# Performance work log

Measured on AMD Instinct MI355X. Metric: run time of the kernel, lower is better.

The kernel has to match this reference:

```python
import jax, jax.numpy as jnp
import numpy as np

NUM_HEADS = 8
LN_EPS = 1e-5


def _ln(x, g, b):
    mu = x.mean(-1, keepdims=True)
    xc = x - mu
    v = (xc * xc).mean(-1, keepdims=True)
    return xc * jax.lax.rsqrt(v + LN_EPS) * g + b


def setup_inputs() -> dict:
    key = jax.random.key(0)
    B, T, D, NI, NT = 16, 512, 256, 85, 77
    L, FF, TH = 2, 1024, 32
    ks = iter(jax.random.split(key, 40))
    def nrm(shape, std):
        return jax.random.normal(next(ks), shape, jnp.float32) * std
    inp = {
        'img_tokens': nrm((B, NI, D), 1.0),
        'text_tokens': nrm((B, NT, D), 1.0),
        'task_tokens': nrm((T, D), 0.02),
        'type_task': nrm((D,), 0.02),
        'type_img': nrm((D,), 0.02),
        'type_txt': nrm((D,), 0.02),
        'in_ln_g': jnp.ones((D,), jnp.float32), 'in_ln_b': jnp.zeros((D,), jnp.float32),
        'Wqkv': nrm((L, 3 * D, D), 1.0 / np.sqrt(D)), 'bqkv': jnp.zeros((L, 3 * D), jnp.float32),
        'Wo': nrm((L, D, D), 1.0 / np.sqrt(D)), 'bo': jnp.zeros((L, D), jnp.float32),
        'ln1_g': jnp.ones((L, D), jnp.float32), 'ln1_b': jnp.zeros((L, D), jnp.float32),
        'ln2_g': jnp.ones((L, D), jnp.float32), 'ln2_b': jnp.zeros((L, D), jnp.float32),
        'W1': nrm((L, FF, D), 1.0 / np.sqrt(D)), 'b1': jnp.zeros((L, FF), jnp.float32),
        'W2': nrm((L, D, FF), 1.0 / np.sqrt(FF)), 'b2': jnp.zeros((L, D), jnp.float32),
        'out_ln_g': jnp.ones((D,), jnp.float32), 'out_ln_b': jnp.zeros((D,), jnp.float32),
        'tw1': nrm((T, TH, D), 1.0 / np.sqrt(D)), 'tb1': jnp.zeros((T, TH), jnp.float32),
        'tw2': nrm((T, TH), 1.0 / np.sqrt(TH)), 'tb2': jnp.zeros((T,), jnp.float32),
        'text_mask': jnp.arange(NT)[None, :] < jax.random.randint(next(ks), (B, 1), 10, NT + 1),
        'labels': jax.random.randint(next(ks), (B, T), -1, 2),
    }
    return inp


def reference(img_tokens, text_tokens, task_tokens, type_task, type_img, type_txt,
              in_ln_g, in_ln_b, Wqkv, bqkv, Wo, bo, ln1_g, ln1_b, ln2_g, ln2_b,
              W1, b1, W2, b2, out_ln_g, out_ln_b, tw1, tb1, tw2, tb2,
              text_mask, labels):
    B, NI, D = img_tokens.shape
    T = task_tokens.shape[0]
    L = Wqkv.shape[0]
    hd = D // NUM_HEADS
    available = labels != -1                                   # (B, T)
    n_avail = available.sum(axis=1)                            # (B,)
    # Route B: stable-sort available task ids to the front (permutation per row)
    order = jnp.argsort((~available).astype(jnp.int32), axis=1, stable=True)  # (B, T)
    task_toks = task_tokens[order] + type_task                 # (B, T, D)
    seq = jnp.concatenate([task_toks, img_tokens + type_img, text_tokens + type_txt], axis=1)
    seq = _ln(seq, in_ln_g, in_ln_b)
    task_pad = jnp.arange(T)[None, :] >= n_avail[:, None]
    pad = jnp.concatenate([task_pad, jnp.zeros((B, NI), bool), ~text_mask], axis=1)
    bias = jnp.where(pad, -1e9, 0.0).astype(seq.dtype)[:, None, None, :]  # key-padding mask
    scale = 1.0 / np.sqrt(hd)
    S = seq.shape[1]
    for l in range(L):  # pre-LN transformer encoder layers (eval mode)
        h = _ln(seq, ln1_g[l], ln1_b[l])
        qkv = h @ Wqkv[l].T + bqkv[l]
        q, k, v = jnp.split(qkv, 3, axis=-1)
        q = q.reshape(B, S, NUM_HEADS, hd)
        k = k.reshape(B, S, NUM_HEADS, hd)
        v = v.reshape(B, S, NUM_HEADS, hd)
        scores = jnp.einsum('bqhd,bkhd->bhqk', q, k) * scale + bias
        attn = jax.nn.softmax(scores, axis=-1)
        o = jnp.einsum('bhqk,bkhd->bqhd', attn, v).reshape(B, S, D)
        seq = seq + o @ Wo[l].T + bo[l]
        h2 = _ln(seq, ln2_g[l], ln2_b[l])
        seq = seq + jax.nn.gelu(h2 @ W1[l].T + b1[l], approximate=False) @ W2[l].T + b2[l]
    task_out = _ln(seq[:, :T], out_ln_g, out_ln_b)             # (B, T, D)
    # undo the per-row permutation so task t's token sits at column t, then
    # apply all per-task towers as one grouped matmul (MoE dispatch/combine)
    y = jnp.zeros_like(task_out).at[jnp.arange(B)[:, None], order].set(task_out)
    hsz = jax.nn.relu(jnp.einsum('btd,thd->bth', y, tw1) + tb1[None])
    out = jnp.einsum('bth,th->bt', hsz, tw2) + tb2[None]
    return jnp.where(available, out, jnp.zeros((), out.dtype))
```

## Files before the change

kernel.cpp:

```cpp
#include <hip/hip_runtime.h>
#include <hip/hip_bf16.h>
#include <math.h>

constexpr int B_  = 16;
constexpr int T_  = 512;
constexpr int D_  = 256;
constexpr int NI_ = 85;
constexpr int NT_ = 77;
constexpr int S_  = T_ + NI_ + NT_;
constexpr int M_  = B_ * S_;
constexpr int FF_ = 1024;
constexpr int TH_ = 32;
constexpr int NH_ = 8;
constexpr int KT_ = 704;
constexpr int NKT_ = KT_ / 64;

constexpr float MASK_NEG = -30000.0f;

constexpr int N_FT = 26;
constexpr int OFF_[N_FT + 1] = {
    0,
    348160,
    663552,
    794624,
    794880,
    795136,
    795392,
    795648,
    795904,
    1189120,
    1190656,
    1321728,
    1322240,
    1322752,
    1323264,
    1323776,
    1324288,
    1848576,
    1850624,
    2374912,
    2375424,
    2375680,
    2375936,
    6570240,
    6586624,
    6603008,
    6603520
};
constexpr int TOTAL_ELEMS = OFF_[N_FT];
constexpr int CONV_BLOCKS = (TOTAL_ELEMS + 511) / 512;

typedef __attribute__((ext_vector_type(8))) short bfrag;
typedef __attribute__((ext_vector_type(4))) float f32x4;

__device__ inline float bf2f(__hip_bfloat16 x) { return __bfloat162float(x); }
__device__ inline __hip_bfloat16 f2bf(float x) { return __float2bfloat16(x); }
__device__ inline float wsum64(float v) {
    #pragma unroll
    for (int m = 32; m >= 1; m >>= 1) v += __shfl_xor(v, m, 64);
    return v;
}
__device__ inline bool is_f32_mode(const void* ln_g_raw) {
    return (*(const unsigned int*)ln_g_raw) == 0x3F800000u;
}

__device__ inline bool tile_dead(int m0, int m1, const int* __restrict__ n_avail) {
    int b = m0 / S_;
    int base = b * S_;
    return (m0 >= base + n_avail[b]) && (m1 <= base + T_);
}

__device__ inline void gload_lds16(const __hip_bfloat16* g, __hip_bfloat16* l) {
#if defined(__has_builtin) && __has_builtin(__builtin_amdgcn_global_load_lds)
    __builtin_amdgcn_global_load_lds(
        (const __attribute__((address_space(1))) unsigned int*)g,
        (__attribute__((address_space(3))) unsigned int*)l, 16, 0, 0);
#else
    *reinterpret_cast<uint4*>(l) = *reinterpret_cast<const uint4*>(g);
#endif
}

__device__ inline float gelu_f(float v) {
    return 0.5f * v * (1.f + erff(v * 0.70710678118654752f));
}

struct Ptrs { const void* p[N_FT]; };

__global__ __launch_bounds__(512) void k_init(Ptrs ptrs, __hip_bfloat16* __restrict__ canon,
                                              const int* __restrict__ labels,
                                              int* __restrict__ inv,
                                              int* __restrict__ n_avail) {
    if (blockIdx.x < CONV_BLOCKS) {
        int idx = blockIdx.x * 512 + threadIdx.x;
        if (idx >= TOTAL_ELEMS) return;
        bool f32 = is_f32_mode(ptrs.p[6]);
        int t = 0;
        #pragma unroll
        for (int i = 1; i < N_FT; i++) if (idx >= OFF_[i]) t = i;
        int local = idx - OFF_[t];
        if (f32) canon[idx] = f2bf(((const float*)ptrs.p[t])[local]);
        else     canon[idx] = ((const __hip_bfloat16*)ptrs.p[t])[local];
    } else {
        __shared__ int sc[T_];
        int b = blockIdx.x - CONV_BLOCKS, t = threadIdx.x;
        int av = (labels[b * T_ + t] != -1) ? 1 : 0;
        sc[t] = av;
        __syncthreads();
        for (int off = 1; off < T_; off <<= 1) {
            int v = sc[t];
            int u = (t >= off) ? sc[t - off] : 0;
            __syncthreads();
            sc[t] = v + u;
            __syncthreads();
        }
        int incl  = sc[t];
        int excl  = incl - av;
        int total = sc[T_ - 1];
        inv[b * T_ + t] = av ? excl : (total + (t - excl));
        if (t == 0) n_avail[b] = total;
    }
}

__global__ void k_build(const __hip_bfloat16* __restrict__ img,
                        const __hip_bfloat16* __restrict__ txt,
                        const __hip_bfloat16* __restrict__ task,
                        const __hip_bfloat16* __restrict__ ty_task,
                        const __hip_bfloat16* __restrict__ ty_img,
                        const __hip_bfloat16* __restrict__ ty_txt,
                        const __hip_bfloat16* __restrict__ g,
                        const __hip_bfloat16* __restrict__ bln,
                        const __hip_bfloat16* __restrict__ g1,
                        const __hip_bfloat16* __restrict__ b1,
                        const void* __restrict__ text_mask,
                        const int* __restrict__ inv,
                        const int* __restrict__ n_avail,
                        float* __restrict__ seq,
                        __hip_bfloat16* __restrict__ h1,
                        float* __restrict__ bias) {
    int blk = blockIdx.x;
    int b = blk / S_, j = blk % S_;
    int lane = threadIdx.x;

    int dest;
    float bias_v;
    const __hip_bfloat16* src;
    const __hip_bfloat16* tvec;
    if (j < T_) {
        dest = inv[b * T_ + j];
        src = task + (size_t)j * D_;
        tvec = ty_task;
        bias_v = (dest >= n_avail[b]) ? MASK_NEG : 0.f;
    } else if (j < T_ + NI_) {
        dest = j;
        src = img + (size_t)(b * NI_ + (j - T_)) * D_;
        tvec = ty_img;
        bias_v = 0.f;
    } else {
        int x2 = j - T_ - NI_;
        dest = j;
        src = txt + (size_t)(b * NT_ + x2) * D_;
        tvec = ty_txt;
        const unsigned char* mb = (const unsigned char*)text_mask;
        bool is_byte = (mb[1] != 0);
        int mv = is_byte ? (int)mb[b * NT_ + x2]
                         : ((const int*)text_mask)[b * NT_ + x2];
        bias_v = mv ? 0.f : MASK_NEG;
    }

    float x[4];
    float s = 0.f, ss = 0.f;
    #pragma unroll
    for (int i = 0; i < 4; i++) {
        int d = lane * 4 + i;
        x[i] = bf2f(src[d]) + bf2f(tvec[d]);
        s += x[i];
        ss += x[i] * x[i];
    }
    s = wsum64(s);
    ss = wsum64(ss);
    float mean = s * (1.f / D_);
    float var  = ss * (1.f / D_) - mean * mean;
    float r    = rsqrtf(fmaxf(var, 0.f) + 1e-5f);

    float y[4];
    float s2 = 0.f, ss2 = 0.f;
    float* orow = seq + ((size_t)b * S_ + dest) * D_;
    #pragma unroll
    for (int i = 0; i < 4; i++) {
        int d = lane * 4 + i;
        y[i] = (x[i] - mean) * r * bf2f(g[d]) + bf2f(bln[d]);
        orow[d] = y[i];
        s2 += y[i];
        ss2 += y[i] * y[i];
    }
    s2 = wsum64(s2);
    ss2 = wsum64(ss2);
    float mean2 = s2 * (1.f / D_);
    float var2  = ss2 * (1.f / D_) - mean2 * mean2;
    float r2    = rsqrtf(fmaxf(var2, 0.f) + 1e-5f);
    __hip_bfloat16 tmp[4];
    #pragma unroll
    for (int i = 0; i < 4; i++) {
        int d = lane * 4 + i;
        tmp[i] = f2bf((y[i] - mean2) * r2 * bf2f(g1[d]) + bf2f(b1[d]));
    }
    *reinterpret_cast<uint2*>(h1 + ((size_t)b * S_ + dest) * D_ + lane * 4) =
        *reinterpret_cast<uint2*>(tmp);
    if (lane == 0) bias[b * S_ + dest] = bias_v;
}

template <int GELU>
__global__ __launch_bounds__(256) void k_gemm(const __hip_bfloat16* __restrict__ A,
                                              const __hip_bfloat16* __restrict__ W,
                                              const __hip_bfloat16* __restrict__ bias,
                                              __hip_bfloat16* __restrict__ Cout,
                                              const int* __restrict__ n_avail,
                                              int Mm, int N, int K) {
    constexpr int HALF = 12288;
    __shared__ __align__(16) __hip_bfloat16 Sh[2 * HALF];
    __hip_bfloat16* Es = Sh;

    int m0 = blockIdx.x * 64;
    if (tile_dead(m0, m0 + 64, n_avail)) return;
    int n0 = blockIdx.y * 128;
    int tid = threadIdx.x;
    int w = tid >> 6, lane = tid & 63;
    int lrow = lane & 15, quad = lane >> 4;
    int swz = lrow & 7;

    f32x4 acc[8] = {};

    int kq = (((tid & 7) ^ ((tid >> 3) & 7)) * 8);
    int arow = tid >> 3;
    const __hip_bfloat16* Ar0 = A + (size_t)min(m0 + arow,      Mm - 1) * K + kq;
    const __hip_bfloat16* Ar1 = A + (size_t)min(m0 + arow + 32, Mm - 1) * K + kq;
    const __hip_bfloat16* Wr[4];
    #pragma unroll
    for (int i = 0; i < 4; i++)
        Wr[i] = W + (size_t)(n0 + ((tid + i * 256) >> 3)) * K + kq;

    const int nsteps = K >> 6;

    {
        __hip_bfloat16* As0 = Sh;
        __hip_bfloat16* Ws0 = Sh + 4096;
        gload_lds16(Ar0, As0 + tid * 8);
        gload_lds16(Ar1, As0 + (tid + 256) * 8);
        #pragma unroll
        for (int i = 0; i < 4; i++) gload_lds16(Wr[i], Ws0 + (tid + i * 256) * 8);
    }
    __syncthreads();

    for (int ks = 0; ks < nsteps; ks++) {
        int curo = (ks & 1) * HALF;
        if (ks + 1 < nsteps) {
            int k1 = (ks + 1) << 6;
            __hip_bfloat16* Asn = Sh + (HALF - curo);
            __hip_bfloat16* Wsn = Asn + 4096;
            gload_lds16(Ar0 + k1, Asn + tid * 8);
            gload_lds16(Ar1 + k1, Asn + (tid + 256) * 8);
            #pragma unroll
            for (int i = 0; i < 4; i++) gload_lds16(Wr[i] + k1, Wsn + (tid + i * 256) * 8);
        }
        __hip_bfloat16* Asc = Sh + curo;
        __hip_bfloat16* Wsc = Asc + 4096;
        #pragma unroll
        for (int ko = 0; ko < 2; ko++) {
            int unit = ((ko * 4 + quad) ^ swz) << 3;
            bfrag af = *reinterpret_cast<const bfrag*>(&Asc[(w * 16 + lrow) * 64 + unit]);
            #pragma unroll
            for (int nt = 0; nt < 8; nt++) {
                bfrag bf = *reinterpret_cast<const bfrag*>(&Wsc[(nt * 16 + lrow) * 64 + unit]);
                acc[nt] = __builtin_amdgcn_mfma_f32_16x16x32_bf16(af, bf, acc[nt], 0, 0, 0);
            }
        }
        __syncthreads();
    }

    #pragma unroll
    for (int nt = 0; nt < 8; nt++) {
        int col = nt * 16 + lrow;
        float bv = bf2f(bias[n0 + col]);
        #pragma unroll
        for (int rg = 0; rg < 4; rg++) {
            int row = w * 16 + quad * 4 + rg;
            float v = acc[nt][rg] + bv;
            if (GELU) v = gelu_f(v);
            Es[row * 136 + col] = f2bf(v);
        }
    }
    __syncthreads();

    #pragma unroll
    for (int i = 0; i < 4; i++) {
        int c = tid + i * 256;
        int row = c >> 4, off = (c & 15) * 8;
        int gm = m0 + row;
        if (gm < Mm) {
            uint4 v4 = *reinterpret_cast<const uint4*>(&Es[row * 136 + off]);
            *reinterpret_cast<uint4*>(&Cout[(size_t)gm * N + n0 + off]) = v4;
        }
    }
}

template <int LNOUT>
__global__ __launch_bounds__(256) void k_ffnmega(const __hip_bfloat16* __restrict__ A,
                                                 const __hip_bfloat16* __restrict__ Wop,
                                                 const __hip_bfloat16* __restrict__ bop,
                                                 const __hip_bfloat16* __restrict__ ln2g,
                                                 const __hip_bfloat16* __restrict__ ln2b,
                                                 const __hip_bfloat16* __restrict__ W1p,
                                                 const __hip_bfloat16* __restrict__ b1p,
                                                 const __hip_bfloat16* __restrict__ W2p,
                                                 const __hip_bfloat16* __restrict__ b2p,
                                                 float* __restrict__ seq,
                                                 const __hip_bfloat16* __restrict__ g1n,
                                                 const __hip_bfloat16* __restrict__ b1n,
                                                 __hip_bfloat16* __restrict__ lnout,
                                                 const int* __restrict__ n_avail) {
    constexpr int PT_OFF  = 0;
    constexpr int WST_OFF = 4096;
    constexpr int HT_OFF  = 20480;
    constexpr int ESTRIDE = 260;
    __shared__ __align__(16) __hip_bfloat16 Sh[28672];

    int m0 = blockIdx.x * 32;
    if (tile_dead(m0, m0 + 32, n_avail)) return;
    int tid = threadIdx.x;
    int w = tid >> 6, lane = tid & 63;
    int lrow = lane & 15, quad = lane >> 4;
    int swz = lrow & 7;
    int kq = ((tid & 7) ^ ((tid >> 3) & 7)) * 8;

    f32x4 acc[2][4] = {};
    {
        const __hip_bfloat16* Ar = A + (size_t)(m0 + (tid >> 3)) * 256 + kq;
        __hip_bfloat16* As = Sh;
        __hip_bfloat16* Ws = Sh + 2048;
        for (int ks = 0; ks < 4; ks++) {
            int k0 = ks << 6;
            if (ks) __syncthreads();
            gload_lds16(Ar + k0, As + tid * 8);
            #pragma unroll
            for (int i = 0; i < 8; i++)
                gload_lds16(Wop + (size_t)((tid + i * 256) >> 3) * 256 + k0 + kq,
                            Ws + (tid + i * 256) * 8);
            __syncthreads();
            #pragma unroll
            for (int ko = 0; ko < 2; ko++) {
                int unit = ((ko * 4 + quad) ^ swz) << 3;
                bfrag af[2], bf[4];
                #pragma unroll
                for (int mt = 0; mt < 2; mt++)
                    af[mt] = *reinterpret_cast<const bfrag*>(&As[(mt * 16 + lrow) * 64 + unit]);
                #pragma unroll
                for (int nt = 0; nt < 4; nt++)
                    bf[nt] = *reinterpret_cast<const bfrag*>(&Ws[(w * 64 + nt * 16 + lrow) * 64 + unit]);
                #pragma unroll
                for (int mt = 0; mt < 2; mt++)
                    #pragma unroll
                    for (int nt = 0; nt < 4; nt++)
                        acc[mt][nt] = __builtin_amdgcn_mfma_f32_16x16x32_bf16(af[mt], bf[nt], acc[mt][nt], 0, 0, 0);
            }
        }
        __syncthreads();
    }

    float* Es = (float*)Sh;
    #pragma unroll
    for (int nt = 0; nt < 4; nt++) {
        int col = w * 64 + nt * 16 + lrow;
        float bv = bf2f(bop[col]);
        #pragma unroll
        for (int mt = 0; mt < 2; mt++)
            #pragma unroll
            for (int rg = 0; rg < 4; rg++)
                Es[(mt * 16 + quad * 4 + rg) * ESTRIDE + col] = acc[mt][nt][rg] + bv;
    }
    __syncthreads();

    int row = tid >> 3, part = tid & 7;
    size_t gm = (size_t)(m0 + row);
    const float* seqrow = seq + gm * 256 + part * 32;
    float t[32];
    float s = 0.f, ss = 0.f;
    #pragma unroll
    for (int j = 0; j < 8; j++) {
        float4 e  = *reinterpret_cast<const float4*>(&Es[row * ESTRIDE + part * 32 + j * 4]);
        float4 r4 = *reinterpret_cast<const float4*>(&seqrow[j * 4]);
        float v0 = e.x + r4.x, v1 = e.y + r4.y, v2 = e.z + r4.z, v3 = e.w + r4.w;
        t[j * 4 + 0] = v0; t[j * 4 + 1] = v1; t[j * 4 + 2] = v2; t[j * 4 + 3] = v3;
        s += v0 + v1 + v2 + v3;
        ss += v0 * v0 + v1 * v1 + v2 * v2 + v3 * v3;
    }
    #pragma unroll
    for (int mm = 4; mm >= 1; mm >>= 1) {
        s  += __shfl_xor(s,  mm, 8);
        ss += __shfl_xor(ss, mm, 8);
    }
    {
        float mean = s * (1.f / 256);
        float var  = ss * (1.f / 256) - mean * mean;
        float r    = rsqrtf(fmaxf(var, 0.f) + 1e-5f);
        __hip_bfloat16* Ht = Sh + HT_OFF;
        #pragma unroll
        for (int jj = 0; jj < 4; jj++) {
            __hip_bfloat16 hb[8];
            #pragma unroll
            for (int k = 0; k < 8; k++) {
                int col = part * 32 + jj * 8 + k;
                hb[k] = f2bf((t[jj * 8 + k] - mean) * r * bf2f(ln2g[col]) + bf2f(ln2b[col]));
            }
            int unit = (part * 4 + jj) ^ (row & 7);
            *reinterpret_cast<uint4*>(&Ht[row * 256 + unit * 8]) =
                *reinterpret_cast<const uint4*>(hb);
        }
    }
    __syncthreads();

    f32x4 acc2[2][4] = {};
    __hip_bfloat16* Wst = Sh + WST_OFF;
    __hip_bfloat16* Pt  = Sh + PT_OFF;
    __hip_bfloat16* Ht  = Sh + HT_OFF;

    for (int c = 0; c < 8; c++) {
        int ff0 = c << 7;
        f32x4 pacc[2][2] = {};
        for (int ks = 0; ks < 4; ks++) {
            if (c | ks) __syncthreads();
            #pragma unroll
            for (int i = 0; i < 4; i++) {
                int u = tid + i * 256;
                gload_lds16(W1p + (size_t)(ff0 + (u >> 3)) * 256 + (ks << 6) + kq,
                            Wst + u * 8);
            }
            __syncthreads();
            #pragma unroll
            for (int ko = 0; ko < 2; ko++) {
                int hunit = ((ks * 8 + ko * 4 + quad) ^ swz) << 3;
                int wunit = ((ko * 4 + quad) ^ swz) << 3;
                bfrag af[2], bf[2];
                #pragma unroll
                for (int mt = 0; mt < 2; mt++)
                    af[mt] = *reinterpret_cast<const bfrag*>(&Ht[(mt * 16 + lrow) * 256 + hunit]);
                #pragma unroll
                for (int nt = 0; nt < 2; nt++)
                    bf[nt] = *reinterpret_cast<const bfrag*>(&Wst[(w * 32 + nt * 16 + lrow) * 64 + wunit]);
                #pragma unroll
                for (int mt = 0; mt < 2; mt++)
                    #pragma unroll
                    for (int nt = 0; nt < 2; nt++)
                        pacc[mt][nt] = __builtin_amdgcn_mfma_f32_16x16x32_bf16(af[mt], bf[nt], pacc[mt][nt], 0, 0, 0);
            }
        }
        __syncthreads();

        #pragma unroll
        for (int mt = 0; mt < 2; mt++)
            #pragma unroll
            for (int nt = 0; nt < 2; nt++)
                #pragma unroll
                for (int rg = 0; rg < 4; rg++) {
                    int prow = mt * 16 + quad * 4 + rg;
                    int pcol = w * 32 + nt * 16 + lrow;
                    float v = pacc[mt][nt][rg] + bf2f(b1p[ff0 + pcol]);
                    v = gelu_f(v);
                    int unit = (pcol >> 3) ^ (prow & 7);
                    Pt[prow * 128 + unit * 8 + (pcol & 7)] = f2bf(v);
                }

        for (int ks2 = 0; ks2 < 2; ks2++) {
            if (ks2) __syncthreads();
            #pragma unroll
            for (int i = 0; i < 8; i++) {
                int u = tid + i * 256;
                gload_lds16(W2p + (size_t)(u >> 3) * 1024 + ff0 + (ks2 << 6) + kq,
                            Wst + u * 8);
            }
            __syncthreads();
            #pragma unroll
            for (int ko = 0; ko < 2; ko++) {
                int punit = ((ks2 * 8 + ko * 4 + quad) ^ swz) << 3;
                int wunit = ((ko * 4 + quad) ^ swz) << 3;
                bfrag af2[2], bf2v[4];
                #pragma unroll
                for (int mt = 0; mt < 2; mt++)
                    af2[mt] = *reinterpret_cast<const bfrag*>(&Pt[(mt * 16 + lrow) * 128 + punit]);
                #pragma unroll
                for (int nt = 0; nt < 4; nt++)
                    bf2v[nt] = *reinterpret_cast<const bfrag*>(&Wst[(w * 64 + nt * 16 + lrow) * 64 + wunit]);
                #pragma unroll
                for (int mt = 0; mt < 2; mt++)
                    #pragma unroll
                    for (int nt = 0; nt < 4; nt++)
                        acc2[mt][nt] = __builtin_amdgcn_mfma_f32_16x16x32_bf16(af2[mt], bf2v[nt], acc2[mt][nt], 0, 0, 0);
            }
        }
    }
    __syncthreads();

    float* Es2 = (float*)Sh;
    #pragma unroll
    for (int nt = 0; nt < 4; nt++) {
        int col = w * 64 + nt * 16 + lrow;
        float bv = bf2f(b2p[col]);
        #pragma unroll
        for (int mt = 0; mt < 2; mt++)
            #pragma unroll
            for (int rg = 0; rg < 4; rg++)
                Es2[(mt * 16 + quad * 4 + rg) * ESTRIDE + col] = acc2[mt][nt][rg] + bv;
    }
    __syncthreads();

    float* seqw = seq + gm * 256 + part * 32;
    float s2 = 0.f, ss2 = 0.f;
    #pragma unroll
    for (int j = 0; j < 8; j++) {
        float4 e = *reinterpret_cast<const float4*>(&Es2[row * ESTRIDE + part * 32 + j * 4]);
        float v0 = t[j * 4 + 0] + e.x, v1 = t[j * 4 + 1] + e.y;
        float v2 = t[j * 4 + 2] + e.z, v3 = t[j * 4 + 3] + e.w;
        t[j * 4 + 0] = v0; t[j * 4 + 1] = v1; t[j * 4 + 2] = v2; t[j * 4 + 3] = v3;
        s2 += v0 + v1 + v2 + v3;
        ss2 += v0 * v0 + v1 * v1 + v2 * v2 + v3 * v3;
        *reinterpret_cast<float4*>(&seqw[j * 4]) = make_float4(v0, v1, v2, v3);
    }
    if (LNOUT) {
        #pragma unroll
        for (int mm = 4; mm >= 1; mm >>= 1) {
            s2  += __shfl_xor(s2,  mm, 8);
            ss2 += __shfl_xor(ss2, mm, 8);
        }
        float mean = s2 * (1.f / 256);
        float var  = ss2 * (1.f / 256) - mean * mean;
        float r    = rsqrtf(fmaxf(var, 0.f) + 1e-5f);
        __hip_bfloat16 ob[32];
        #pragma unroll
        for (int j = 0; j < 32; j++) {
            int col = part * 32 + j;
            ob[j] = f2bf((t[j] - mean) * r * bf2f(g1n[col]) + bf2f(b1n[col]));
        }
        #pragma unroll
        for (int j = 0; j < 4; j++)
            *reinterpret_cast<uint4*>(&lnout[gm * 256 + part * 32 + j * 8]) =
                *reinterpret_cast<const uint4*>(&ob[j * 8]);
    }
}

__global__ __launch_bounds__(256) void k_fattn(const __hip_bfloat16* __restrict__ qkv,
                                               const float* __restrict__ bias,
                                               const int* __restrict__ n_avail,
                                               __hip_bfloat16* __restrict__ out) {
    __shared__ __align__(16) __hip_bfloat16 Vt[2][32 * 72];
    __shared__ __align__(16) __hip_bfloat16 Ps[4][32 * 72];
    __shared__ float Bs[KT_];
    __shared__ int alive[NKT_];
    __shared__ int tlist[NKT_ + 1];
    __shared__ int nact_s;
    int b = blockIdx.z, h = blockIdx.y;
    int q0b = blockIdx.x * 128;
    if (q0b >= n_avail[b] && q0b + 128 <= T_) return;
    int tid = threadIdx.x;
    int wave = tid >> 6, lane = tid & 63;
    int lrow = lane & 15, quad = lane >> 4;
    int q0 = q0b + wave * 32;

    const float scale = 0.17677669529663687f;
    const __hip_bfloat16* base = qkv + (size_t)b * S_ * 768;
    const float* brow = bias + b * S_;

    if (tid < NKT_) alive[tid] = 0;
    __syncthreads();
    for (int i = tid; i < KT_; i += 256) {
        float v = (i < S_) ? brow[i] : MASK_NEG;
        Bs[i] = v;
        if (v != MASK_NEG) alive[i >> 6] = 1;
    }
    __syncthreads();
    if (tid == 0) {
        int n = 0;
        for (int t = 0; t < NKT_; t++) if (alive[t]) tlist[n++] = t;
        if (n == 0) { tlist[0] = 0; n = 1; }
        tlist[n] = tlist[n - 1];
        nact_s = n;
    }
    __syncthreads();
    int nact = nact_s;

    bfrag qf[2];
    {
        int qr0 = min(q0 + lrow, S_ - 1);
        int qr1 = min(q0 + 16 + lrow, S_ - 1);
        qf[0] = *reinterpret_cast<const bfrag*>(base + (size_t)qr0 * 768 + h * 32 + quad * 8);
        qf[1] = *reinterpret_cast<const bfrag*>(base + (size_t)qr1 * 768 + h * 32 + quad * 8);
    }

    bfrag ones_f;
    #pragma unroll
    for (int i = 0; i < 8; i++) ((short*)&ones_f)[i] = (short)0x3F80;

    float m[2][4];
    #pragma unroll
    for (int qh = 0; qh < 2; qh++)
        #pragma unroll
        for (int rg = 0; rg < 4; rg++) m[qh][rg] = -3e38f;
    f32x4 Lacc[2] = {};
    f32x4 O[2][2] = {};

    int skey = lane;
    int sd   = wave * 8;

    bfrag kf_cur[4], vv_cur;
    {
        int k0 = tlist[0] * 64;
        #pragma unroll
        for (int nt = 0; nt < 4; nt++) {
            int kr = min(k0 + nt * 16 + lrow, S_ - 1);
            kf_cur[nt] = *reinterpret_cast<const bfrag*>(base + (size_t)kr * 768 + 256 + h * 32 + quad * 8);
        }
        int kr = min(k0 + skey, S_ - 1);
        vv_cur = *reinterpret_cast<const bfrag*>(base + (size_t)kr * 768 + 512 + h * 32 + sd);
    }

    for (int i = 0; i < nact; i++) {
        int k0 = tlist[i] * 64;
        __hip_bfloat16* vb = Vt[i & 1];

        #pragma unroll
        for (int j = 0; j < 8; j++) vb[(sd + j) * 72 + skey] = ((const __hip_bfloat16*)&vv_cur)[j];
        __syncthreads();

        bfrag kf_nxt[4], vv_nxt;
        {
            int kb = tlist[i + 1] * 64;
            #pragma unroll
            for (int nt = 0; nt < 4; nt++) {
                int kr = min(kb + nt * 16 + lrow, S_ - 1);
                kf_nxt[nt] = *reinterpret_cast<const bfrag*>(base + (size_t)kr * 768 + 256 + h * 32 + quad * 8);
            }
            int kr = min(kb + skey, S_ - 1);
            vv_nxt = *reinterpret_cast<const bfrag*>(base + (size_t)kr * 768 + 512 + h * 32 + sd);
        }

        f32x4 sc[2][4];
        #pragma unroll
        for (int nt = 0; nt < 4; nt++) {
            float bv = Bs[k0 + nt * 16 + lrow];
            #pragma unroll
            for (int qh = 0; qh < 2; qh++) {
                f32x4 z = {};
                sc[qh][nt] = __builtin_amdgcn_mfma_f32_16x16x32_bf16(qf[qh], kf_cur[nt], z, 0, 0, 0);
                #pragma unroll
                for (int rg = 0; rg < 4; rg++) sc[qh][nt][rg] = sc[qh][nt][rg] * scale + bv;
            }
        }

        #pragma unroll
        for (int qh = 0; qh < 2; qh++) {
            float alpha[4];
            #pragma unroll
            for (int rg = 0; rg < 4; rg++) {
                float rm = fmaxf(fmaxf(sc[qh][0][rg], sc[qh][1][rg]), fmaxf(sc[qh][2][rg], sc[qh][3][rg]));
                #pragma unroll
                for (int mm2 = 1; mm2 <= 8; mm2 <<= 1) rm = fmaxf(rm, __shfl_xor(rm, mm2, 64));
                float mn = fmaxf(m[qh][rg], rm);
                alpha[rg] = __expf(m[qh][rg] - mn);
                m[qh][rg] = mn;
                #pragma unroll
                for (int nt = 0; nt < 4; nt++) sc[qh][nt][rg] = __expf(sc[qh][nt][rg] - mn);
            }
            #pragma unroll
            for (int rg = 0; rg < 4; rg++) {
                O[qh][0][rg] *= alpha[rg];
                O[qh][1][rg] *= alpha[rg];
                Lacc[qh][rg] *= alpha[rg];
            }
            #pragma unroll
            for (int nt = 0; nt < 4; nt++)
                #pragma unroll
                for (int rg = 0; rg < 4; rg++)
                    Ps[wave][(qh * 16 + quad * 4 + rg) * 72 + nt * 16 + lrow] = f2bf(sc[qh][nt][rg]);
        }

        #pragma unroll
        for (int qh = 0; qh < 2; qh++) {
            bfrag ap0 = *reinterpret_cast<const bfrag*>(&Ps[wave][(qh * 16 + lrow) * 72 + quad * 8]);
            bfrag ap1 = *reinterpret_cast<const bfrag*>(&Ps[wave][(qh * 16 + lrow) * 72 + 32 + quad * 8]);
            #pragma unroll
            for (int dt = 0; dt < 2; dt++) {
                bfrag bv0 = *reinterpret_cast<const bfrag*>(&vb[(dt * 16 + lrow) * 72 + quad * 8]);
                bfrag bv1 = *reinterpret_cast<const bfrag*>(&vb[(dt * 16 + lrow) * 72 + 32 + quad * 8]);
                O[qh][dt] = __builtin_amdgcn_mfma_f32_16x16x32_bf16(ap0, bv0, O[qh][dt], 0, 0, 0);
                O[qh][dt] = __builtin_amdgcn_mfma_f32_16x16x32_bf16(ap1, bv1, O[qh][dt], 0, 0, 0);
            }
            Lacc[qh] = __builtin_amdgcn_mfma_f32_16x16x32_bf16(ap0, ones_f, Lacc[qh], 0, 0, 0);
            Lacc[qh] = __builtin_amdgcn_mfma_f32_16x16x32_bf16(ap1, ones_f, Lacc[qh], 0, 0, 0);
        }

        #pragma unroll
        for (int nt = 0; nt < 4; nt++) kf_cur[nt] = kf_nxt[nt];
        vv_cur = vv_nxt;
    }

    #pragma unroll
    for (int qh = 0; qh < 2; qh++)
        #pragma unroll
        for (int rg = 0; rg < 4; rg++) {
            int qrow = q0 + qh * 16 + quad * 4 + rg;
            if (qrow < S_) {
                float invl = 1.f / Lacc[qh][rg];
                #pragma unroll
                for (int dt = 0; dt < 2; dt++)
                    out[((size_t)b * S_ + qrow) * D_ + h * 32 + dt * 16 + lrow] = f2bf(O[qh][dt][rg] * invl);
            }
        }
}

__global__ __launch_bounds__(256) void k_final(const float* __restrict__ seq,
                                               const int* __restrict__ inv,
                                               const int* __restrict__ labels,
                                               const __hip_bfloat16* __restrict__ g,
                                               const __hip_bfloat16* __restrict__ bb,
                                               const __hip_bfloat16* __restrict__ tw1,
                                               const __hip_bfloat16* __restrict__ tb1,
                                               const __hip_bfloat16* __restrict__ tw2,
                                               const __hip_bfloat16* __restrict__ tb2,
                                               const void* __restrict__ ln_g_raw,
                                               void* __restrict__ out) {
    int idx = blockIdx.x;
    int t = idx >> 4, b = idx & 15;
    int tid = threadIdx.x;
    bool f32o = is_f32_mode(ln_g_raw);

    int lab = labels[b * T_ + t];
    if (lab == -1) {
        if (tid == 0) {
            if (f32o) ((float*)out)[b * T_ + t] = 0.f;
            else      ((__hip_bfloat16*)out)[b * T_ + t] = f2bf(0.f);
        }
        return;
    }

    __shared__ float y[D_];
    __shared__ float hb[TH_];
    __shared__ float rs[4], rq[4];

    int row = inv[b * T_ + t];
    float x = seq[((size_t)b * S_ + row) * D_ + tid];
    float s1 = wsum64(x);
    float s2 = wsum64(x * x);
    int w = tid >> 6, lane = tid & 63;
    if (lane == 0) { rs[w] = s1; rq[w] = s2; }
    __syncthreads();
    float fs = rs[0] + rs[1] + rs[2] + rs[3];
    float fq = rq[0] + rq[1] + rq[2] + rq[3];
    float mean = fs * (1.f / D_);
    float var  = fq * (1.f / D_) - mean * mean;
    float r    = rsqrtf(fmaxf(var, 0.f) + 1e-5f);
    y[tid] = (x - mean) * r * bf2f(g[tid]) + bf2f(bb[tid]);
    __syncthreads();

    int hh = tid >> 3, part = tid & 7;
    const uint4* w4 = reinterpret_cast<const uint4*>(tw1 + ((size_t)t * TH_ + hh) * D_ + part * 32);
    float acc = 0.f;
    #pragma unroll
    for (int i = 0; i < 4; i++) {
        uint4 kv = w4[i];
        unsigned int wd[4] = {kv.x, kv.y, kv.z, kv.w};
        #pragma unroll
        for (int j2 = 0; j2 < 4; j2++) {
            unsigned int lo = wd[j2] << 16, hi = wd[j2] & 0xffff0000u;
            float flo, fhi;
            __builtin_memcpy(&flo, &lo, 4);
            __builtin_memcpy(&fhi, &hi, 4);
            acc += y[part * 32 + i * 8 + j2 * 2] * flo;
            acc += y[part * 32 + i * 8 + j2 * 2 + 1] * fhi;
        }
    }
    #pragma unroll
    for (int mm = 4; mm >= 1; mm >>= 1) acc += __shfl_down(acc, mm, 8);
    if (part == 0) {
        float hz = acc + bf2f(tb1[t * TH_ + hh]);
        hz = fmaxf(hz, 0.f);
        hb[hh] = hz * bf2f(tw2[t * TH_ + hh]);
    }
    __syncthreads();
    if (tid == 0) {
        float o = bf2f(tb2[t]);
        #pragma unroll
        for (int i = 0; i < TH_; i++) o += hb[i];
        if (f32o) ((float*)out)[b * T_ + t] = o;
        else      ((__hip_bfloat16*)out)[b * T_ + t] = f2bf(o);
    }
}

extern "C" void kernel_launch(void* const* d_in, const int* in_sizes, int n_in,
                              void* d_out, int out_size, void* d_ws, size_t ws_size,
                              hipStream_t stream) {
    const void* tmask  = d_in[26];
    const int*  labels = (const int*)d_in[27];

    char* p = (char*)d_ws;
    auto alloc = [&](size_t bytes) {
        char* r = p;
        p += (bytes + 255) & ~size_t(255);
        return r;
    };
    __hip_bfloat16* canon  = (__hip_bfloat16*)alloc(sizeof(__hip_bfloat16) * (size_t)TOTAL_ELEMS);
    int*            inv     = (int*)alloc(sizeof(int) * B_ * T_);
    int*            n_avail = (int*)alloc(sizeof(int) * B_);
    float*          bias    = (float*)alloc(sizeof(float) * M_);
    float*          seqF    = (float*)alloc(sizeof(float) * (size_t)M_ * D_);
    __hip_bfloat16* bufA    = (__hip_bfloat16*)alloc(sizeof(__hip_bfloat16) * (size_t)M_ * D_);
    __hip_bfloat16* bufBig  = (__hip_bfloat16*)alloc(sizeof(__hip_bfloat16) * (size_t)M_ * FF_);

    Ptrs ptrs;
    for (int i = 0; i < N_FT; i++) ptrs.p[i] = d_in[i];
    hipLaunchKernelGGL(k_init, dim3(CONV_BLOCKS + B_), dim3(512), 0, stream,
                       ptrs, canon, labels, inv, n_avail);

    const __hip_bfloat16* img      = canon + OFF_[0];
    const __hip_bfloat16* txt      = canon + OFF_[1];
    const __hip_bfloat16* task     = canon + OFF_[2];
    const __hip_bfloat16* ty_task  = canon + OFF_[3];
    const __hip_bfloat16* ty_img   = canon + OFF_[4];
    const __hip_bfloat16* ty_txt   = canon + OFF_[5];
    const __hip_bfloat16* in_ln_g  = canon + OFF_[6];
    const __hip_bfloat16* in_ln_b  = canon + OFF_[7];
    const __hip_bfloat16* Wqkv     = canon + OFF_[8];
    const __hip_bfloat16* bqkv     = canon + OFF_[9];
    const __hip_bfloat16* Wo       = canon + OFF_[10];
    const __hip_bfloat16* bo       = canon + OFF_[11];
    const __hip_bfloat16* ln1_g    = canon + OFF_[12];
    const __hip_bfloat16* ln1_b    = canon + OFF_[13];
    const __hip_bfloat16* ln2_g    = canon + OFF_[14];
    const __hip_bfloat16* ln2_b    = canon + OFF_[15];
    const __hip_bfloat16* W1       = canon + OFF_[16];
    const __hip_bfloat16* b1       = canon + OFF_[17];
    const __hip_bfloat16* W2       = canon + OFF_[18];
    const __hip_bfloat16* b2       = canon + OFF_[19];
    const __hip_bfloat16* out_ln_g = canon + OFF_[20];
    const __hip_bfloat16* out_ln_b = canon + OFF_[21];
    const __hip_bfloat16* tw1      = canon + OFF_[22];
    const __hip_bfloat16* tb1      = canon + OFF_[23];
    const __hip_bfloat16* tw2      = canon + OFF_[24];
    const __hip_bfloat16* tb2      = canon + OFF_[25];

    hipLaunchKernelGGL(k_build, dim3(B_ * S_), dim3(64), 0, stream,
                       img, txt, task, ty_task, ty_img, ty_txt, in_ln_g, in_ln_b,
                       ln1_g, ln1_b, tmask, inv, n_avail, seqF, bufA, bias);

    const int mtiles = (M_ + 63) / 64;
    const int rtiles = M_ / 32;
    const int qtiles = (S_ + 127) / 128;

    for (int l = 0; l < 2; l++) {
        hipLaunchKernelGGL((k_gemm<0>), dim3(mtiles, 6), dim3(256), 0, stream,
                           bufA, Wqkv + (size_t)l * 3 * D_ * D_, bqkv + l * 3 * D_,
                           bufBig, n_avail, M_, 3 * D_, D_);
        hipLaunchKernelGGL(k_fattn, dim3(qtiles, NH_, B_), dim3(256), 0, stream,
                           bufBig, bias, n_avail, bufA);
        if (l == 0) {
            hipLaunchKernelGGL((k_ffnmega<1>), dim3(rtiles), dim3(256), 0, stream,
                               bufA,
                               Wo + (size_t)l * D_ * D_, bo + l * D_,
                               ln2_g + l * D_, ln2_b + l * D_,
                               W1 + (size_t)l * FF_ * D_, b1 + l * FF_,
                               W2 + (size_t)l * D_ * FF_, b2 + l * D_,
                               seqF, ln1_g + 1 * D_, ln1_b + 1 * D_, bufA, n_avail);
        } else {
            hipLaunchKernelGGL((k_ffnmega<0>), dim3(rtiles), dim3(256), 0, stream,
                               bufA,
                               Wo + (size_t)l * D_ * D_, bo + l * D_,
                               ln2_g + l * D_, ln2_b + l * D_,
                               W1 + (size_t)l * FF_ * D_, b1 + l * FF_,
                               W2 + (size_t)l * D_ * FF_, b2 + l * D_,
                               seqF, (const __hip_bfloat16*)nullptr,
                               (const __hip_bfloat16*)nullptr,
                               (__hip_bfloat16*)nullptr, n_avail);
        }
    }

    hipLaunchKernelGGL(k_final, dim3(T_ * B_), dim3(256), 0, stream,
                       seqF, inv, labels, out_ln_g, out_ln_b,
                       tw1, tb1, tw2, tb2, d_in[6], d_out);
}
```

Measured before the change: 366.1 us.

## Double-buffer weight staging in fused out-proj/FFN kernel to overlap loads with MFMA

Reworks the k_ffnmega weight staging into a uniform 128x64 tile loader with two LDS buffers. The next tile (Wo, W1 or W2) is prefetched while the current one feeds the MFMAs, which leaves one barrier per step instead of two. The A tile is loaded once into the Ht region, and the output-column mapping is split into two 128-column halves to match the smaller tiles. The cost is more, smaller stages and a more intricate buffer/barrier schedule, including the GELU-to-Pt handoff at the end of each W1 chunk.

```diff
diff --git a/kernel.cpp b/kernel.cpp
--- a/kernel.cpp
+++ b/kernel.cpp
@@ -318,7 +318,6 @@
                                                  const __hip_bfloat16* __restrict__ b1n,
                                                  __hip_bfloat16* __restrict__ lnout,
                                                  const int* __restrict__ n_avail) {
-    constexpr int PT_OFF  = 0;
     constexpr int WST_OFF = 4096;
     constexpr int HT_OFF  = 20480;
     constexpr int ESTRIDE = 260;
@@ -330,52 +329,70 @@
     int w = tid >> 6, lane = tid & 63;
     int lrow = lane & 15, quad = lane >> 4;
     int swz = lrow & 7;
-    int kq = ((tid & 7) ^ ((tid >> 3) & 7)) * 8;
-
+
+    __hip_bfloat16* Pt  = Sh;
+    __hip_bfloat16* Wst = Sh + WST_OFF;
+    __hip_bfloat16* Ht  = Sh + HT_OFF;
+
+    auto stageW = [&](const __hip_bfloat16* srcbase, int rowstride, __hip_bfloat16* dst) {
+        #pragma unroll
+        for (int i = 0; i < 4; i++) {
+            int u = tid + i * 256;
+            int r = u >> 3, c = u & 7;
+            gload_lds16(srcbase + (size_t)r * rowstride + ((c ^ (r & 7)) << 3), dst + u * 8);
+        }
+    };
+
+    #pragma unroll
+    for (int i = 0; i < 4; i++) {
+        int u = tid + i * 256;
+        int r = u >> 5, c = u & 31;
+        gload_lds16(A + (size_t)(m0 + r) * 256 + ((c ^ (r & 7)) << 3), Ht + u * 8);
+    }
+    stageW(Wop, 256, Wst);
+    __syncthreads();
+
+    int bufp = 0;
     f32x4 acc[2][4] = {};
-    {
-        const __hip_bfloat16* Ar = A + (size_t)(m0 + (tid >> 3)) * 256 + kq;
-        __hip_bfloat16* As = Sh;
-        __hip_bfloat16* Ws = Sh + 2048;
-        for (int ks = 0; ks < 4; ks++) {
-            int k0 = ks << 6;
-            if (ks) __syncthreads();
-            gload_lds16(Ar + k0, As + tid * 8);
-            #pragma unroll
-            for (int i = 0; i < 8; i++)
-                gload_lds16(Wop + (size_t)((tid + i * 256) >> 3) * 256 + k0 + kq,
-                            Ws + (tid + i * 256) * 8);
-            __syncthreads();
-            #pragma unroll
-            for (int ko = 0; ko < 2; ko++) {
-                int unit = ((ko * 4 + quad) ^ swz) << 3;
-                bfrag af[2], bf[4];
-                #pragma unroll
-                for (int mt = 0; mt < 2; mt++)
-                    af[mt] = *reinterpret_cast<const bfrag*>(&As[(mt * 16 + lrow) * 64 + unit]);
-                #pragma unroll
-                for (int nt = 0; nt < 4; nt++)
-                    bf[nt] = *reinterpret_cast<const bfrag*>(&Ws[(w * 64 + nt * 16 + lrow) * 64 + unit]);
-                #pragma unroll
-                for (int mt = 0; mt < 2; mt++)
-                    #pragma unroll
-                    for (int nt = 0; nt < 4; nt++)
-                        acc[mt][nt] = __builtin_amdgcn_mfma_f32_16x16x32_bf16(af[mt], bf[nt], acc[mt][nt], 0, 0, 0);
-            }
+    for (int s = 0; s < 8; s++) {
+        if (s < 7) {
+            int s1 = s + 1;
+            stageW(Wop + ((s1 >> 2) * 128) * 256 + (s1 & 3) * 64, 256,
+                   Wst + (bufp ^ 1) * 8192);
+        }
+        int ks = s & 3, h = s >> 2;
+        __hip_bfloat16* wb = Wst + bufp * 8192;
+        #pragma unroll
+        for (int ko = 0; ko < 2; ko++) {
+            int aunit = (ks * 8 + ko * 4 + quad) ^ swz;
+            int wunit = (ko * 4 + quad) ^ swz;
+            bfrag af[2], bf[2];
+            #pragma unroll
+            for (int mt = 0; mt < 2; mt++)
+                af[mt] = *reinterpret_cast<const bfrag*>(&Ht[((mt * 16 + lrow) * 32 + aunit) * 8]);
+            #pragma unroll
+            for (int nt = 0; nt < 2; nt++)
+                bf[nt] = *reinterpret_cast<const bfrag*>(&wb[((w * 32 + nt * 16 + lrow) * 8 + wunit) * 8]);
+            #pragma unroll
+            for (int mt = 0; mt < 2; mt++)
+                #pragma unroll
+                for (int nt = 0; nt < 2; nt++)
+                    acc[mt][h * 2 + nt] = __builtin_amdgcn_mfma_f32_16x16x32_bf16(af[mt], bf[nt], acc[mt][h * 2 + nt], 0, 0, 0);
         }
         __syncthreads();
+        bufp ^= 1;
     }
 
     float* Es = (float*)Sh;
     #pragma unroll
-    for (int nt = 0; nt < 4; nt++) {
-        int col = w * 64 + nt * 16 + lrow;
+    for (int j = 0; j < 4; j++) {
+        int col = (j >> 1) * 128 + w * 32 + (j & 1) * 16 + lrow;
         float bv = bf2f(bop[col]);
         #pragma unroll
         for (int mt = 0; mt < 2; mt++)
             #pragma unroll
             for (int rg = 0; rg < 4; rg++)
-                Es[(mt * 16 + quad * 4 + rg) * ESTRIDE + col] = acc[mt][nt][rg] + bv;
+                Es[(mt * 16 + quad * 4 + rg) * ESTRIDE + col] = acc[mt][j][rg] + bv;
     }
     __syncthreads();
 
@@ -402,7 +419,6 @@
         float mean = s * (1.f / 256);
         float var  = ss * (1.f / 256) - mean * mean;
         float r    = rsqrtf(fmaxf(var, 0.f) + 1e-5f);
-        __hip_bfloat16* Ht = Sh + HT_OFF;
         #pragma unroll
         for (int jj = 0; jj < 4; jj++) {
             __hip_bfloat16 hb[8];
@@ -417,98 +433,97 @@
         }
     }
     __syncthreads();
+    stageW(W1p, 256, Wst);
+    __syncthreads();
+    bufp = 0;
 
     f32x4 acc2[2][4] = {};
-    __hip_bfloat16* Wst = Sh + WST_OFF;
-    __hip_bfloat16* Pt  = Sh + PT_OFF;
-    __hip_bfloat16* Ht  = Sh + HT_OFF;
-
     for (int c = 0; c < 8; c++) {
         int ff0 = c << 7;
         f32x4 pacc[2][2] = {};
         for (int ks = 0; ks < 4; ks++) {
-            if (c | ks) __syncthreads();
-            #pragma unroll
-            for (int i = 0; i < 4; i++) {
-                int u = tid + i * 256;
-                gload_lds16(W1p + (size_t)(ff0 + (u >> 3)) * 256 + (ks << 6) + kq,
-                            Wst + u * 8);
-            }
-            __syncthreads();
+            if (ks < 3)
+                stageW(W1p + (size_t)ff0 * 256 + (ks + 1) * 64, 256, Wst + (bufp ^ 1) * 8192);
+            else
+                stageW(W2p + ff0, 1024, Wst + (bufp ^ 1) * 8192);
+            __hip_bfloat16* wb = Wst + bufp * 8192;
             #pragma unroll
             for (int ko = 0; ko < 2; ko++) {
-                int hunit = ((ks * 8 + ko * 4 + quad) ^ swz) << 3;
-                int wunit = ((ko * 4 + quad) ^ swz) << 3;
+                int hunit = (ks * 8 + ko * 4 + quad) ^ swz;
+                int wunit = (ko * 4 + quad) ^ swz;
                 bfrag af[2], bf[2];
                 #pragma unroll
                 for (int mt = 0; mt < 2; mt++)
-                    af[mt] = *reinterpret_cast<const bfrag*>(&Ht[(mt * 16 + lrow) * 256 + hunit]);
+                    af[mt] = *reinterpret_cast<const bfrag*>(&Ht[((mt * 16 + lrow) * 32 + hunit) * 8]);
                 #pragma unroll
                 for (int nt = 0; nt < 2; nt++)
-                    bf[nt] = *reinterpret_cast<const bfrag*>(&Wst[(w * 32 + nt * 16 + lrow) * 64 + wunit]);
+                    bf[nt] = *reinterpret_cast<const bfrag*>(&wb[((w * 32 + nt * 16 + lrow) * 8 + wunit) * 8]);
                 #pragma unroll
                 for (int mt = 0; mt < 2; mt++)
                     #pragma unroll
                     for (int nt = 0; nt < 2; nt++)
                         pacc[mt][nt] = __builtin_amdgcn_mfma_f32_16x16x32_bf16(af[mt], bf[nt], pacc[mt][nt], 0, 0, 0);
             }
-        }
-        __syncthreads();
-
-        #pragma unroll
-        for (int mt = 0; mt < 2; mt++)
-            #pragma unroll
-            for (int nt = 0; nt < 2; nt++)
-                #pragma unroll
-                for (int rg = 0; rg < 4; rg++) {
-                    int prow = mt * 16 + quad * 4 + rg;
-                    int pcol = w * 32 + nt * 16 + lrow;
-                    float v = pacc[mt][nt][rg] + bf2f(b1p[ff0 + pcol]);
-                    v = gelu_f(v);
-                    int unit = (pcol >> 3) ^ (prow & 7);
-                    Pt[prow * 128 + unit * 8 + (pcol & 7)] = f2bf(v);
-                }
-
-        for (int ks2 = 0; ks2 < 2; ks2++) {
-            if (ks2) __syncthreads();
-            #pragma unroll
-            for (int i = 0; i < 8; i++) {
-                int u = tid + i * 256;
-                gload_lds16(W2p + (size_t)(u >> 3) * 1024 + ff0 + (ks2 << 6) + kq,
-                            Wst + u * 8);
-            }
-            __syncthreads();
-            #pragma unroll
-            for (int ko = 0; ko < 2; ko++) {
-                int punit = ((ks2 * 8 + ko * 4 + quad) ^ swz) << 3;
-                int wunit = ((ko * 4 + quad) ^ swz) << 3;
-                bfrag af2[2], bf2v[4];
-                #pragma unroll
-                for (int mt = 0; mt < 2; mt++)
-                    af2[mt] = *reinterpret_cast<const bfrag*>(&Pt[(mt * 16 + lrow) * 128 + punit]);
-                #pragma unroll
-                for (int nt = 0; nt < 4; nt++)
-                    bf2v[nt] = *reinterpret_cast<const bfrag*>(&Wst[(w * 64 + nt * 16 + lrow) * 64 + wunit]);
+            if (ks == 3) {
                 #pragma unroll
                 for (int mt = 0; mt < 2; mt++)
                     #pragma unroll
-                    for (int nt = 0; nt < 4; nt++)
-                        acc2[mt][nt] = __builtin_amdgcn_mfma_f32_16x16x32_bf16(af2[mt], bf2v[nt], acc2[mt][nt], 0, 0, 0);
-            }
-        }
-    }
-    __syncthreads();
+                    for (int nt = 0; nt < 2; nt++)
+                        #pragma unroll
+                        for (int rg = 0; rg < 4; rg++) {
+                            int prow = mt * 16 + quad * 4 + rg;
+                            int pcol = w * 32 + nt * 16 + lrow;
+                            float v = pacc[mt][nt][rg] + bf2f(b1p[ff0 + pcol]);
+                            v = gelu_f(v);
+                            int unit = (pcol >> 3) ^ (prow & 7);
+                            Pt[prow * 128 + unit * 8 + (pcol & 7)] = f2bf(v);
+                        }
+            }
+            __syncthreads();
+            bufp ^= 1;
+        }
+        for (int tt = 0; tt < 4; tt++) {
+            if (tt < 3) {
+                int t1 = tt + 1;
+                stageW(W2p + (size_t)((t1 >> 1) * 128) * 1024 + ff0 + (t1 & 1) * 64, 1024,
+                       Wst + (bufp ^ 1) * 8192);
+            } else if (c < 7) {
+                stageW(W1p + (size_t)(ff0 + 128) * 256, 256, Wst + (bufp ^ 1) * 8192);
+            }
+            int h = tt >> 1, ks2 = tt & 1;
+            __hip_bfloat16* wb = Wst + bufp * 8192;
+            #pragma unroll
+            for (int ko = 0; ko < 2; ko++) {
+                int punit = (ks2 * 8 + ko * 4 + quad) ^ swz;
+                int wunit = (ko * 4 + quad) ^ swz;
+                bfrag af2[2], bf2v[2];
+                #pragma unroll
+                for (int mt = 0; mt < 2; mt++)
+                    af2[mt] = *reinterpret_cast<const bfrag*>(&Pt[((mt * 16 + lrow) * 16 + punit) * 8]);
+                #pragma unroll
+                for (int nt = 0; nt < 2; nt++)
+                    bf2v[nt] = *reinterpret_cast<const bfrag*>(&wb[((w * 32 + nt * 16 + lrow) * 8 + wunit) * 8]);
+                #pragma unroll
+                for (int mt = 0; mt < 2; mt++)
+                    #pragma unroll
+                    for (int nt = 0; nt < 2; nt++)
+                        acc2[mt][h * 2 + nt] = __builtin_amdgcn_mfma_f32_16x16x32_bf16(af2[mt], bf2v[nt], acc2[mt][h * 2 + nt], 0, 0, 0);
+            }
+            __syncthreads();
+            bufp ^= 1;
+        }
+    }
 
     float* Es2 = (float*)Sh;
     #pragma unroll
-    for (int nt = 0; nt < 4; nt++) {
-        int col = w * 64 + nt * 16 + lrow;
+    for (int j = 0; j < 4; j++) {
+        int col = (j >> 1) * 128 + w * 32 + (j & 1) * 16 + lrow;
         float bv = bf2f(b2p[col]);
         #pragma unroll
         for (int mt = 0; mt < 2; mt++)
             #pragma unroll
             for (int rg = 0; rg < 4; rg++)
-                Es2[(mt * 16 + quad * 4 + rg) * ESTRIDE + col] = acc2[mt][nt][rg] + bv;
+                Es2[(mt * 16 + quad * 4 + rg) * ESTRIDE + col] = acc2[mt][j][rg] + bv;
     }
     __syncthreads();
 
```

After: 362.8 us (median of 3 runs). About the same (-0.9%).

## Load FFN weight fragments directly from global and stage full GELU activations in LDS

Applied to the files above, without the earlier changes.

The fused out-proj+LN+FFN kernel stops staging weight tiles through shared memory with barriers. Each wavefront now reads its MFMA B-fragments straight from global memory (L2-cached weights). The FF1 stage is repartitioned so each wave owns two 128-column chunks, and the full 32x1024 GELU output is kept in LDS before a single FF2 pass. This removes many __syncthreads and LDS staging copies. In exchange the global loads are uncoalesced, 16-byte row-strided reads, and shared memory use grows to 80KB, which may lower occupancy.

```diff
diff --git a/kernel.cpp b/kernel.cpp
--- a/kernel.cpp
+++ b/kernel.cpp
@@ -318,11 +318,9 @@
                                                  const __hip_bfloat16* __restrict__ b1n,
                                                  __hip_bfloat16* __restrict__ lnout,
                                                  const int* __restrict__ n_avail) {
-    constexpr int PT_OFF  = 0;
-    constexpr int WST_OFF = 4096;
-    constexpr int HT_OFF  = 20480;
+    constexpr int HT_OFF  = 32768;
     constexpr int ESTRIDE = 260;
-    __shared__ __align__(16) __hip_bfloat16 Sh[28672];
+    __shared__ __align__(16) __hip_bfloat16 Sh[40960];
 
     int m0 = blockIdx.x * 32;
     if (tile_dead(m0, m0 + 32, n_avail)) return;
@@ -330,40 +328,26 @@
     int w = tid >> 6, lane = tid & 63;
     int lrow = lane & 15, quad = lane >> 4;
     int swz = lrow & 7;
-    int kq = ((tid & 7) ^ ((tid >> 3) & 7)) * 8;
+
+    __hip_bfloat16* Pt = Sh;
+    __hip_bfloat16* Ht = Sh + HT_OFF;
 
     f32x4 acc[2][4] = {};
     {
-        const __hip_bfloat16* Ar = A + (size_t)(m0 + (tid >> 3)) * 256 + kq;
-        __hip_bfloat16* As = Sh;
-        __hip_bfloat16* Ws = Sh + 2048;
-        for (int ks = 0; ks < 4; ks++) {
-            int k0 = ks << 6;
-            if (ks) __syncthreads();
-            gload_lds16(Ar + k0, As + tid * 8);
-            #pragma unroll
-            for (int i = 0; i < 8; i++)
-                gload_lds16(Wop + (size_t)((tid + i * 256) >> 3) * 256 + k0 + kq,
-                            Ws + (tid + i * 256) * 8);
-            __syncthreads();
-            #pragma unroll
-            for (int ko = 0; ko < 2; ko++) {
-                int unit = ((ko * 4 + quad) ^ swz) << 3;
-                bfrag af[2], bf[4];
-                #pragma unroll
-                for (int mt = 0; mt < 2; mt++)
-                    af[mt] = *reinterpret_cast<const bfrag*>(&As[(mt * 16 + lrow) * 64 + unit]);
-                #pragma unroll
-                for (int nt = 0; nt < 4; nt++)
-                    bf[nt] = *reinterpret_cast<const bfrag*>(&Ws[(w * 64 + nt * 16 + lrow) * 64 + unit]);
-                #pragma unroll
-                for (int mt = 0; mt < 2; mt++)
-                    #pragma unroll
-                    for (int nt = 0; nt < 4; nt++)
-                        acc[mt][nt] = __builtin_amdgcn_mfma_f32_16x16x32_bf16(af[mt], bf[nt], acc[mt][nt], 0, 0, 0);
-            }
-        }
-        __syncthreads();
+        const __hip_bfloat16* Aw = A + (size_t)m0 * 256;
+        const __hip_bfloat16* Ww = Wop + (size_t)(w * 64) * 256;
+        #pragma unroll
+        for (int ks8 = 0; ks8 < 8; ks8++) {
+            int ko = ks8 * 32 + quad * 8;
+            bfrag af0 = *reinterpret_cast<const bfrag*>(Aw + (size_t)lrow * 256 + ko);
+            bfrag af1 = *reinterpret_cast<const bfrag*>(Aw + (size_t)(16 + lrow) * 256 + ko);
+            #pragma unroll
+            for (int nt = 0; nt < 4; nt++) {
+                bfrag bf = *reinterpret_cast<const bfrag*>(Ww + (size_t)(nt * 16 + lrow) * 256 + ko);
+                acc[0][nt] = __builtin_amdgcn_mfma_f32_16x16x32_bf16(af0, bf, acc[0][nt], 0, 0, 0);
+                acc[1][nt] = __builtin_amdgcn_mfma_f32_16x16x32_bf16(af1, bf, acc[1][nt], 0, 0, 0);
+            }
+        }
     }
 
     float* Es = (float*)Sh;
@@ -402,7 +386,6 @@
         float mean = s * (1.f / 256);
         float var  = ss * (1.f / 256) - mean * mean;
         float r    = rsqrtf(fmaxf(var, 0.f) + 1e-5f);
-        __hip_bfloat16* Ht = Sh + HT_OFF;
         #pragma unroll
         for (int jj = 0; jj < 4; jj++) {
             __hip_bfloat16 hb[8];
@@ -418,82 +401,60 @@
     }
     __syncthreads();
 
-    f32x4 acc2[2][4] = {};
-    __hip_bfloat16* Wst = Sh + WST_OFF;
-    __hip_bfloat16* Pt  = Sh + PT_OFF;
-    __hip_bfloat16* Ht  = Sh + HT_OFF;
-
-    for (int c = 0; c < 8; c++) {
-        int ff0 = c << 7;
-        f32x4 pacc[2][2] = {};
-        for (int ks = 0; ks < 4; ks++) {
-            if (c | ks) __syncthreads();
-            #pragma unroll
-            for (int i = 0; i < 4; i++) {
-                int u = tid + i * 256;
-                gload_lds16(W1p + (size_t)(ff0 + (u >> 3)) * 256 + (ks << 6) + kq,
-                            Wst + u * 8);
-            }
-            __syncthreads();
-            #pragma unroll
-            for (int ko = 0; ko < 2; ko++) {
-                int hunit = ((ks * 8 + ko * 4 + quad) ^ swz) << 3;
-                int wunit = ((ko * 4 + quad) ^ swz) << 3;
-                bfrag af[2], bf[2];
+    for (int i = 0; i < 2; i++) {
+        int c = w * 2 + i;
+        const __hip_bfloat16* W1c = W1p + (size_t)(c * 128) * 256;
+        f32x4 pacc[2][8];
+        #pragma unroll
+        for (int mt = 0; mt < 2; mt++)
+            #pragma unroll
+            for (int nt = 0; nt < 8; nt++)
                 #pragma unroll
-                for (int mt = 0; mt < 2; mt++)
-                    af[mt] = *reinterpret_cast<const bfrag*>(&Ht[(mt * 16 + lrow) * 256 + hunit]);
-                #pragma unroll
-                for (int nt = 0; nt < 2; nt++)
-                    bf[nt] = *reinterpret_cast<const bfrag*>(&Wst[(w * 32 + nt * 16 + lrow) * 64 + wunit]);
-                #pragma unroll
-                for (int mt = 0; mt < 2; mt++)
-                    #pragma unroll
-                    for (int nt = 0; nt < 2; nt++)
-                        pacc[mt][nt] = __builtin_amdgcn_mfma_f32_16x16x32_bf16(af[mt], bf[nt], pacc[mt][nt], 0, 0, 0);
-            }
-        }
-        __syncthreads();
-
-        #pragma unroll
-        for (int mt = 0; mt < 2; mt++)
-            #pragma unroll
-            for (int nt = 0; nt < 2; nt++)
+                for (int e = 0; e < 4; e++) pacc[mt][nt][e] = 0.f;
+        #pragma unroll
+        for (int ks8 = 0; ks8 < 8; ks8++) {
+            int aunit = (ks8 * 4 + quad) ^ swz;
+            bfrag af0 = *reinterpret_cast<const bfrag*>(&Ht[lrow * 256 + aunit * 8]);
+            bfrag af1 = *reinterpret_cast<const bfrag*>(&Ht[(16 + lrow) * 256 + aunit * 8]);
+            int ko = ks8 * 32 + quad * 8;
+            #pragma unroll
+            for (int nt = 0; nt < 8; nt++) {
+                bfrag bf = *reinterpret_cast<const bfrag*>(W1c + (size_t)(nt * 16 + lrow) * 256 + ko);
+                pacc[0][nt] = __builtin_amdgcn_mfma_f32_16x16x32_bf16(af0, bf, pacc[0][nt], 0, 0, 0);
+                pacc[1][nt] = __builtin_amdgcn_mfma_f32_16x16x32_bf16(af1, bf, pacc[1][nt], 0, 0, 0);
+            }
+        }
+        #pragma unroll
+        for (int nt = 0; nt < 8; nt++) {
+            int pcol = c * 128 + nt * 16 + lrow;
+            float bv = bf2f(b1p[pcol]);
+            #pragma unroll
+            for (int mt = 0; mt < 2; mt++)
                 #pragma unroll
                 for (int rg = 0; rg < 4; rg++) {
                     int prow = mt * 16 + quad * 4 + rg;
-                    int pcol = w * 32 + nt * 16 + lrow;
-                    float v = pacc[mt][nt][rg] + bf2f(b1p[ff0 + pcol]);
-                    v = gelu_f(v);
+                    float v = gelu_f(pacc[mt][nt][rg] + bv);
                     int unit = (pcol >> 3) ^ (prow & 7);
-                    Pt[prow * 128 + unit * 8 + (pcol & 7)] = f2bf(v);
+                    Pt[prow * 1024 + unit * 8 + (pcol & 7)] = f2bf(v);
                 }
-
-        for (int ks2 = 0; ks2 < 2; ks2++) {
-            if (ks2) __syncthreads();
-            #pragma unroll
-            for (int i = 0; i < 8; i++) {
-                int u = tid + i * 256;
-                gload_lds16(W2p + (size_t)(u >> 3) * 1024 + ff0 + (ks2 << 6) + kq,
-                            Wst + u * 8);
-            }
-            __syncthreads();
-            #pragma unroll
-            for (int ko = 0; ko < 2; ko++) {
-                int punit = ((ks2 * 8 + ko * 4 + quad) ^ swz) << 3;
-                int wunit = ((ko * 4 + quad) ^ swz) << 3;
-                bfrag af2[2], bf2v[4];
-                #pragma unroll
-                for (int mt = 0; mt < 2; mt++)
-                    af2[mt] = *reinterpret_cast<const bfrag*>(&Pt[(mt * 16 + lrow) * 128 + punit]);
-                #pragma unroll
-                for (int nt = 0; nt < 4; nt++)
-                    bf2v[nt] = *reinterpret_cast<const bfrag*>(&Wst[(w * 64 + nt * 16 + lrow) * 64 + wunit]);
-                #pragma unroll
-                for (int mt = 0; mt < 2; mt++)
-                    #pragma unroll
-                    for (int nt = 0; nt < 4; nt++)
-                        acc2[mt][nt] = __builtin_amdgcn_mfma_f32_16x16x32_bf16(af2[mt], bf2v[nt], acc2[mt][nt], 0, 0, 0);
+        }
+    }
+    __syncthreads();
+
+    f32x4 acc2[2][4] = {};
+    {
+        const __hip_bfloat16* W2w = W2p + (size_t)(w * 64) * 1024;
+        #pragma unroll 4
+        for (int ks2 = 0; ks2 < 32; ks2++) {
+            int punit = (ks2 * 4 + quad) ^ swz;
+            bfrag af0 = *reinterpret_cast<const bfrag*>(&Pt[lrow * 1024 + punit * 8]);
+            bfrag af1 = *reinterpret_cast<const bfrag*>(&Pt[(16 + lrow) * 1024 + punit * 8]);
+            int ko = ks2 * 32 + quad * 8;
+            #pragma unroll
+            for (int nt = 0; nt < 4; nt++) {
+                bfrag bf = *reinterpret_cast<const bfrag*>(W2w + (size_t)(nt * 16 + lrow) * 1024 + ko);
+                acc2[0][nt] = __builtin_amdgcn_mfma_f32_16x16x32_bf16(af0, bf, acc2[0][nt], 0, 0, 0);
+                acc2[1][nt] = __builtin_amdgcn_mfma_f32_16x16x32_bf16(af1, bf, acc2[1][nt], 0, 0, 0);
             }
         }
     }
```

Measured after the change: 434.7 us. 1.19x slower.
